# Performance work log

Measured on AMD Instinct MI355X. Metric: run time of the kernel, lower is better.

## Reference

```python
import math
import jax, jax.numpy as jnp
import numpy as np

D_MODEL, D_HEAD, BLOCK, B, N = 1024, 128, 2048, 4, 2048
# mode_gate('wake') blend weights (omega_lang, omega_grav)
OMEGA_LANG, OMEGA_GRAV = 0.7, 0.3


def setup_inputs() -> dict:
    key = jax.random.key(0)
    kx, kq, kk, kv, kl = jax.random.split(key, 5)
    x = jax.random.normal(kx, (B, N, D_MODEL), dtype=jnp.float32)
    # nn.Linear(d_model, d_head, bias=False) -> store as [d_model, d_head] for x @ W
    s = 1.0 / math.sqrt(D_MODEL)
    Wq = jax.random.uniform(kq, (D_MODEL, D_HEAD), jnp.float32, -s, s)
    Wk = jax.random.uniform(kk, (D_MODEL, D_HEAD), jnp.float32, -s, s)
    Wv = jax.random.uniform(kv, (D_MODEL, D_HEAD), jnp.float32, -s, s)
    # L_grav = eye*0.3 + randn*0.05
    L_grav = jnp.eye(D_HEAD, dtype=jnp.float32) * 0.3 \
        + jax.random.normal(kl, (D_HEAD, D_HEAD), dtype=jnp.float32) * 0.05
    return {"x": x, "Wq": Wq, "Wk": Wk, "Wv": Wv, "L_grav": L_grav}


def reference(x, Wq, Wk, Wv, L_grav):
    b, n, _ = x.shape
    d_head = Wq.shape[1]
    q = x @ Wq          # [b, n, d]
    k = x @ Wk          # [b, n, d]
    v = x @ Wv          # [b, n, d]
    mask = jnp.tril(jnp.ones((n, n), dtype=bool))  # causal, broadcast over batch

    # lang_attention: scaled dot-product with causal softmax
    scores = jnp.einsum('bqd,bkd->bqk', q, k) / math.sqrt(d_head)
    scores = jnp.where(mask, scores, -jnp.inf)
    a_lang = jax.nn.softmax(scores, axis=-1)       # [b, n, n]

    # grav_attention: Gaussian kernel on Mahalanobis-transformed keys y = k @ L_grav,
    # sigma = sqrt(d_head); masked + row-normalized (non-softmax).
    y = k @ L_grav                                  # [b, n, d]
    sq = jnp.sum(y * y, axis=-1)                    # [b, n]
    gram = jnp.einsum('bqd,bkd->bqk', y, y)         # [b, n, n]
    dist2 = jnp.maximum(sq[:, :, None] + sq[:, None, :] - 2.0 * gram, 0.0)
    kern = jnp.exp(-dist2 / (2.0 * d_head))         # sigma^2 = d_head
    kern = jnp.where(mask, kern, 0.0)
    a_grav = kern / (jnp.sum(kern, axis=-1, keepdims=True) + 1e-8)

    a = OMEGA_LANG * a_lang + OMEGA_GRAV * a_grav   # mode='wake' gate blend
    return a @ v                                    # [b, n, d_head]
```

## Files before the change

### kernel.cpp

```cpp
#include <hip/hip_runtime.h>
#include <hip/hip_bf16.h>
#include <math.h>

typedef __attribute__((ext_vector_type(8))) short short8;
typedef __attribute__((ext_vector_type(4))) short s16x4;
typedef __attribute__((ext_vector_type(4))) float f32x4;

#define SEQ 2048
#define DH 128


__device__ __forceinline__ short f2bf(float f) {
    union { float f; unsigned u; } v; v.f = f;
    unsigned r = v.u + 0x7fffu + ((v.u >> 16) & 1u);
    return (short)(r >> 16);
}
__device__ __forceinline__ float bf2f(short s) {
    union { unsigned u; float f; } v; v.u = ((unsigned)(unsigned short)s) << 16;
    return v.f;
}

__device__ __forceinline__ void gll16(const void* g, void* l) {
    __builtin_amdgcn_global_load_lds(
        (const __attribute__((address_space(1))) unsigned int*)g,
        (__attribute__((address_space(3))) unsigned int*)l, 16, 0, 0);
}

__global__ __launch_bounds__(256) void wt_kernel(
    const float* __restrict__ Wq, const float* __restrict__ Wk, const float* __restrict__ Wv,
    short* __restrict__ Wt2)
{
    const int t = threadIdx.x;
    const int m  = blockIdx.x >> 4;
    const int ks = blockIdx.x & 15;
    const float* W = m == 0 ? Wq : (m == 1 ? Wk : Wv);
    short* dst = Wt2 + ((size_t)(m * 16 + ks) * 1024) * 8;
    #pragma unroll
    for (int j = 0; j < 4; j++) {
        const int idx = t * 4 + j;
        const int ctile = idx >> 7;
        const int kc = (idx >> 6) & 1;
        const int gg = (idx >> 4) & 3;
        const int cc = idx & 15;
        const int col = ctile * 16 + cc;
        const int kb = ks * 64 + kc * 32 + gg * 8;
        short8 h;
        #pragma unroll
        for (int e = 0; e < 8; e++) h[e] = f2bf(W[(size_t)(kb + e) * 128 + col]);
        *(short8*)&dst[idx * 8] = h;
    }
}

__global__ __launch_bounds__(256) void proj_kernel(
    const float* __restrict__ x, const short* __restrict__ Wt2,
    short* __restrict__ Qh, short* __restrict__ Kh, short* __restrict__ Vh)
{
    __shared__ short Xs[2048];
    __shared__ short Ws[8192];
    const int t = threadIdx.x;
    const int w = t >> 6, l = t & 63;
    const int c = l & 15, g = l >> 4;
    const int bid = blockIdx.x;
    const int m = bid % 3;
    const int row0 = (bid / 3) * 32;
    const short* Wm = Wt2 + (size_t)m * 16 * 1024 * 8;

    const int xr = t >> 3;
    const int xk = (t & 7) * 8;
    const int xIdx = ((xr >> 4) * 2 + (xk >> 5)) * 64 + ((xk >> 3) & 3) * 16 + (xr & 15);

    const int rt = w & 1;
    const int ct4 = (w >> 1) * 4;
    f32x4 acc[4];
    #pragma unroll
    for (int nt = 0; nt < 4; nt++) acc[nt] = (f32x4)0.f;

    for (int ks = 0; ks < 16; ks++) {
        __syncthreads();
        const short* wsrc = Wm + ((size_t)ks * 1024 + w * 256 + l) * 8;
        #pragma unroll
        for (int j = 0; j < 4; j++)
            gll16(wsrc + j * 64 * 8, (void*)&Ws[(w * 256 + j * 64) * 8]);
        {
            const float* xp = &x[(size_t)(row0 + xr) * 1024 + ks * 64 + xk];
            const float4 a = *(const float4*)xp;
            const float4 b = *(const float4*)(xp + 4);
            short8 h;
            h[0] = f2bf(a.x); h[1] = f2bf(a.y); h[2] = f2bf(a.z); h[3] = f2bf(a.w);
            h[4] = f2bf(b.x); h[5] = f2bf(b.y); h[6] = f2bf(b.z); h[7] = f2bf(b.w);
            *(short8*)&Xs[xIdx * 8] = h;
        }
        __syncthreads();
        #pragma unroll
        for (int kc = 0; kc < 2; kc++) {
            const short8 af = *(const short8*)&Xs[((rt * 2 + kc) * 64 + l) * 8];
            #pragma unroll
            for (int nt = 0; nt < 4; nt++) {
                const short8 bf = *(const short8*)&Ws[(((ct4 + nt) * 2 + kc) * 64 + l) * 8];
                acc[nt] = __builtin_amdgcn_mfma_f32_16x16x32_bf16(af, bf, acc[nt], 0, 0, 0);
            }
        }
    }
    short* Out = m == 0 ? Qh : (m == 1 ? Kh : Vh);
    #pragma unroll
    for (int nt = 0; nt < 4; nt++)
        #pragma unroll
        for (int r = 0; r < 4; r++) {
            const int R = row0 + rt * 16 + 4 * g + r;
            const int col = (ct4 + nt) * 16 + c;
            const short hv = f2bf(acc[nt][r]);
            if (m == 2)
                Out[(size_t)R * 128 + col] = hv;
            else
                Out[(size_t)(R >> 6) * 8192 + ((col >> 3) * 64 + (R & 63)) * 8 + (col & 7)] = hv;
        }
}

__global__ __launch_bounds__(256) void y_kernel(
    const short* __restrict__ Kh, const float* __restrict__ L,
    short* __restrict__ Yh, float* __restrict__ SQ)
{
    __shared__ float Ls[128 * 128];
    __shared__ short Ks[16][128];
    const int t = threadIdx.x;
    const int row0 = blockIdx.x * 16;
    #pragma unroll
    for (int j = 0; j < 16; j++) {
        int lin = t + j * 256;
        ((float4*)Ls)[lin] = ((const float4*)L)[lin];
    }
    {
        int r = t >> 4, ch = t & 15;
        const int R = row0 + r;
        *(short8*)&Ks[r][ch * 8] =
            *(const short8*)&Kh[(size_t)(R >> 6) * 8192 + (ch * 64 + (R & 63)) * 8];
    }
    __syncthreads();
    const int rl = t >> 4, c4 = (t & 15) * 4;
    float acc[8] = {};
    for (int d = 0; d < 128; d++) {
        const float kd = bf2f(Ks[rl][d]);
        const float4 l0 = *(const float4*)&Ls[d * 128 + c4];
        const float4 l1 = *(const float4*)&Ls[d * 128 + c4 + 64];
        acc[0] += kd * l0.x; acc[1] += kd * l0.y; acc[2] += kd * l0.z; acc[3] += kd * l0.w;
        acc[4] += kd * l1.x; acc[5] += kd * l1.y; acc[6] += kd * l1.z; acc[7] += kd * l1.w;
    }
    const int R = row0 + rl;
    s16x4 h0, h1;
    float s = 0.f;
    #pragma unroll
    for (int j = 0; j < 4; j++) {
        short h = f2bf(acc[j]);     float rv = bf2f(h); s += rv * rv; h0[j] = h;
        short g = f2bf(acc[j + 4]); float gv = bf2f(g); s += gv * gv; h1[j] = g;
    }
    const size_t base = (size_t)(R >> 6) * 8192 + (size_t)(R & 63) * 8;
    *(s16x4*)&Yh[base + (c4 >> 3) * 512 + (c4 & 7)] = h0;
    *(s16x4*)&Yh[base + ((c4 + 64) >> 3) * 512 + (c4 & 7)] = h1;
    for (int off = 1; off < 16; off <<= 1) s += __shfl_xor(s, off);
    if ((t & 15) == 0) SQ[R] = s;
}

__global__ __launch_bounds__(256) void vt_kernel(
    const short* __restrict__ Vh, short* __restrict__ Vf)
{
    __shared__ short Ls[64][72];
    const int t = threadIdx.x;
    const int b  = blockIdx.x >> 6;
    const int nb = (blockIdx.x >> 1) & 31;
    const int db = blockIdx.x & 1;
    const int n0 = nb * 64, d0 = db * 64;
    const short* Vb = Vh + (size_t)b * SEQ * 128;
    short* Vfb = Vf + (size_t)b * SEQ * 128;
    #pragma unroll
    for (int i = 0; i < 2; i++) {
        int row = (t >> 3) + 32 * i;
        int ch = t & 7;
        *(short8*)&Ls[row][ch * 8] = *(const short8*)&Vb[(size_t)(n0 + row) * 128 + d0 + ch * 8];
    }
    __syncthreads();
    #pragma unroll
    for (int i = 0; i < 2; i++) {
        int dd = (t >> 3) + 32 * i;
        int nc = t & 7;
        short8 v;
        #pragma unroll
        for (int j = 0; j < 8; j++) v[j] = Ls[nc * 8 + j][dd];
        *(short8*)&Vfb[(size_t)(n0 >> 6) * 8192 + (nc * 128 + d0 + dd) * 8] = v;
    }
}

__global__ __launch_bounds__(256, 2) void attn_kernel(
    const short* __restrict__ Qf, const short* __restrict__ Kf,
    const short* __restrict__ Yf, const short* __restrict__ Vf,
    const float* __restrict__ SQv,
    float* __restrict__ OL, float* __restrict__ OG,
    float* __restrict__ LS, float* __restrict__ GS)
{
    __shared__ __align__(16) short Bs[2][8192];
    __shared__ __align__(16) short Vs[2][8192];
    __shared__ __align__(16) short P[4 * 2 * 512];
    __shared__ float Rs[32];
    float* Obuf = (float*)&Bs[0][0];

    const int t = threadIdx.x;
    const int w = t >> 6, l = t & 63;
    const int c = l & 15, g = l >> 4;
    const int qh = w & 1, kh = w >> 1;
    const int wbase = t & 192;
    const int bid = blockIdx.x;
    const int b = bid & 3;
    const int grav = (bid >> 2) & 1;
    const int s = (bid >> 3) & 1;
    const int jp = bid >> 4;

    const size_t fb = (size_t)b * SEQ * 128;
    const short* Ap = (grav ? Yf : Qf) + fb;
    const short* Bp = (grav ? Yf : Kf) + fb;
    const short* Vp = Vf + fb;
    const float* SQb = SQv + b * SEQ;

    const float CL = 0.12751743f;
    const float CG = -0.0056355275f;

    for (int m = 0; m < 2; m++) {
        const int qt = m ? 63 - jp : jp;
        const int q0 = qt * 32;
        const int nkt = (qt + 2) >> 1;

        __syncthreads();

        short8 qf[4];
        const size_t qtb = (size_t)(qt >> 1) * 8192;
        const int qlocal = (qt & 1) * 32 + qh * 16 + c;
        #pragma unroll
        for (int kc = 0; kc < 4; kc++)
            qf[kc] = *(const short8*)&Ap[qtb + ((kc * 4 + g) * 64 + qlocal) * 8];

        float sqq[4];
        if (grav) {
            #pragma unroll
            for (int r = 0; r < 4; r++)
                sqq[r] = SQb[q0 + qh * 16 + 4 * g + r];
        }

        f32x4 acc[8];
        #pragma unroll
        for (int dt = 0; dt < 8; dt++) acc[dt] = (f32x4)0.f;
        float rsum[4] = {};

        if (s < nkt) {
            {
                const short* bs0 = Bp + (size_t)s * 8192;
                const short* vs0 = Vp + (size_t)s * 8192;
                #pragma unroll
                for (int j = 0; j < 4; j++)
                    gll16(bs0 + (j * 256 + t) * 8, (void*)&Bs[0][(j * 256 + wbase) * 8]);
                #pragma unroll
                for (int j = 0; j < 4; j++)
                    gll16(vs0 + (j * 256 + t) * 8, (void*)&Vs[0][(j * 256 + wbase) * 8]);
            }
            int cur = 0, pb = 0;
            for (int tt = s; tt < nkt; tt += 2, cur ^= 1, pb ^= 1) {
                __syncthreads();
                if (tt + 2 < nkt) {
                    const short* bsn = Bp + (size_t)(tt + 2) * 8192;
                    const short* vsn = Vp + (size_t)(tt + 2) * 8192;
                    #pragma unroll
                    for (int j = 0; j < 4; j++)
                        gll16(bsn + (j * 256 + t) * 8, (void*)&Bs[cur ^ 1][(j * 256 + wbase) * 8]);
                    #pragma unroll
                    for (int j = 0; j < 4; j++)
                        gll16(vsn + (j * 256 + t) * 8, (void*)&Vs[cur ^ 1][(j * 256 + wbase) * 8]);
                }
                const int k0 = tt * 64;
                short* Pp = P + (w * 2 + pb) * 512;

                #pragma unroll
                for (int kt = 0; kt < 2; kt++) {
                    f32x4 sc = (f32x4)0.f;
                    #pragma unroll
                    for (int kc = 0; kc < 4; kc++) {
                        const short8 bf = *(const short8*)
                            &Bs[cur][((kc * 4 + g) * 64 + kh * 32 + kt * 16 + c) * 8];
                        sc = __builtin_amdgcn_mfma_f32_16x16x32_bf16(qf[kc], bf, sc, 0, 0, 0);
                    }
                    const int key = k0 + kh * 32 + kt * 16 + c;
                    const float sqkv = grav ? SQb[key] : 0.f;
                    #pragma unroll
                    for (int r = 0; r < 4; r++) {
                        const int qrow = q0 + qh * 16 + 4 * g + r;
                        float p = 0.f;
                        if (key <= qrow) {
                            if (grav) {
                                float d2 = sqq[r] + sqkv - 2.f * sc[r];
                                d2 = fmaxf(d2, 0.f);
                                p = __builtin_amdgcn_exp2f(d2 * CG);
                            } else {
                                p = __builtin_amdgcn_exp2f(sc[r] * CL);
                            }
                        }
                        const short ph = f2bf(p);
                        rsum[r] += bf2f(ph);
                        const int row = 4 * g + r;
                        Pp[row * 32 + ((kt * 16 + c) ^ (g << 3))] = ph;
                    }
                }

                const short8 pf = *(const short8*)&Pp[c * 32 + 8 * (g ^ ((c >> 2) & 3))];
                #pragma unroll
                for (int dt = 0; dt < 8; dt++) {
                    const short8 vf = *(const short8*)
                        &Vs[cur][((kh * 4 + g) * 128 + dt * 16 + c) * 8];
                    acc[dt] = __builtin_amdgcn_mfma_f32_16x16x32_bf16(pf, vf, acc[dt], 0, 0, 0);
                }
            }
        }

        __syncthreads();
        for (int i = t; i < 32 * 132; i += 256) Obuf[i] = 0.f;
        if (t < 32) Rs[t] = 0.f;
        __syncthreads();

        #pragma unroll
        for (int dt = 0; dt < 8; dt++)
            #pragma unroll
            for (int r = 0; r < 4; r++)
                atomicAdd(&Obuf[(qh * 16 + 4 * g + r) * 132 + dt * 16 + c], acc[dt][r]);

        #pragma unroll
        for (int r = 0; r < 4; r++) {
            float v = rsum[r];
            v += __shfl_xor(v, 1); v += __shfl_xor(v, 2);
            v += __shfl_xor(v, 4); v += __shfl_xor(v, 8);
            rsum[r] = v;
        }
        if (c == 0) {
            #pragma unroll
            for (int r = 0; r < 4; r++)
                atomicAdd(&Rs[qh * 16 + 4 * g + r], rsum[r]);
        }
        __syncthreads();

        float* Op = (grav ? OG : OL) + fb + (size_t)q0 * 128;
        #pragma unroll
        for (int i = 0; i < 16; i++) {
            const int v2 = t + 256 * i;
            atomicAdd(&Op[v2], Obuf[(v2 >> 7) * 132 + (v2 & 127)]);
        }
        if (t < 32) atomicAdd(&(grav ? GS : LS)[b * SEQ + q0 + t], Rs[t]);
    }
}

__global__ __launch_bounds__(256) void finalize_kernel(
    float* __restrict__ out, const float* __restrict__ OG,
    const float* __restrict__ LS, const float* __restrict__ GS)
{
    const int i4 = blockIdx.x * 256 + threadIdx.x;
    float4 o = ((float4*)out)[i4];
    const float4 gv = ((const float4*)OG)[i4];
    const int row = i4 >> 5;
    const float wl = 0.7f / LS[row];
    const float wg = 0.3f / (GS[row] + 1e-8f);
    o.x = o.x * wl + gv.x * wg;
    o.y = o.y * wl + gv.y * wg;
    o.z = o.z * wl + gv.z * wg;
    o.w = o.w * wl + gv.w * wg;
    ((float4*)out)[i4] = o;
}

extern "C" void kernel_launch(void* const* d_in, const int* in_sizes, int n_in,
                              void* d_out, int out_size, void* d_ws, size_t ws_size,
                              hipStream_t stream) {
    const float* x  = (const float*)d_in[0];
    const float* Wq = (const float*)d_in[1];
    const float* Wk = (const float*)d_in[2];
    const float* Wv = (const float*)d_in[3];
    const float* Lg = (const float*)d_in[4];

    char* ws = (char*)d_ws;
    short* Qh  = (short*)(ws + 0);
    short* Kh  = (short*)(ws + 2097152);
    short* Vh  = (short*)(ws + 4194304);
    short* Yh  = (short*)(ws + 6291456);
    short* Vf  = (short*)(ws + 8388608);
    short* Wt2 = (short*)(ws + 10485760);
    float* SQv = (float*)(ws + 11272192);
    float* LS  = (float*)(ws + 11304960);
    float* GS  = (float*)(ws + 11337728);
    float* OG  = (float*)(ws + 11370496);
    float* OL  = (float*)d_out;

    hipMemsetAsync(d_out, 0, 4194304, stream);
    hipMemsetAsync((void*)LS, 0, 65536, stream);
    hipMemsetAsync((void*)OG, 0, 4194304, stream);

    wt_kernel<<<48, 256, 0, stream>>>(Wq, Wk, Wv, Wt2);
    proj_kernel<<<768, 256, 0, stream>>>(x, Wt2, Qh, Kh, Vh);
    y_kernel<<<512, 256, 0, stream>>>(Kh, Lg, Yh, SQv);
    vt_kernel<<<256, 256, 0, stream>>>(Vh, Vf);
    attn_kernel<<<512, 256, 0, stream>>>(Qh, Kh, Yh, Vf, SQv, OL, OG, LS, GS);
    finalize_kernel<<<1024, 256, 0, stream>>>((float*)d_out, OG, LS, GS);
}
```

Measured before the change: 127.9 us.

## Drop LDS staging of K/V tiles, load fragments directly from global, one q-tile per block

The attention kernel no longer double-buffers K/Y and V tiles into shared memory with async global-to-LDS loads. Each wave now reads its MFMA operand fragments straight from global memory (relying on cache) and drops the per-iteration block barrier. The paired light/heavy q-tile loop is replaced by one q-tile per block with twice as many blocks, heaviest tiles first, and the 2-blocks-per-CU launch bound is removed. The smaller LDS footprint may allow more resident blocks, but every wave now fetches K/V redundantly from L2 without an explicit prefetch, so load latency is less hidden.

```diff
diff --git a/kernel.cpp b/kernel.cpp
--- a/kernel.cpp
+++ b/kernel.cpp
@@ -189,29 +189,28 @@
     }
 }
 
-__global__ __launch_bounds__(256, 2) void attn_kernel(
+__global__ __launch_bounds__(256) void attn_kernel(
     const short* __restrict__ Qf, const short* __restrict__ Kf,
     const short* __restrict__ Yf, const short* __restrict__ Vf,
     const float* __restrict__ SQv,
     float* __restrict__ OL, float* __restrict__ OG,
     float* __restrict__ LS, float* __restrict__ GS)
 {
-    __shared__ __align__(16) short Bs[2][8192];
-    __shared__ __align__(16) short Vs[2][8192];
     __shared__ __align__(16) short P[4 * 2 * 512];
+    __shared__ float Obuf[32][132];
     __shared__ float Rs[32];
-    float* Obuf = (float*)&Bs[0][0];
 
     const int t = threadIdx.x;
     const int w = t >> 6, l = t & 63;
     const int c = l & 15, g = l >> 4;
     const int qh = w & 1, kh = w >> 1;
-    const int wbase = t & 192;
     const int bid = blockIdx.x;
     const int b = bid & 3;
     const int grav = (bid >> 2) & 1;
     const int s = (bid >> 3) & 1;
-    const int jp = bid >> 4;
+    const int qt = 63 - (bid >> 4);
+    const int q0 = qt * 32;
+    const int nkt = (qt + 2) >> 1;
 
     const size_t fb = (size_t)b * SEQ * 128;
     const short* Ap = (grav ? Yf : Qf) + fb;
@@ -222,133 +221,115 @@
     const float CL = 0.12751743f;
     const float CG = -0.0056355275f;
 
-    for (int m = 0; m < 2; m++) {
-        const int qt = m ? 63 - jp : jp;
-        const int q0 = qt * 32;
-        const int nkt = (qt + 2) >> 1;
-
-        __syncthreads();
-
-        short8 qf[4];
-        const size_t qtb = (size_t)(qt >> 1) * 8192;
-        const int qlocal = (qt & 1) * 32 + qh * 16 + c;
-        #pragma unroll
-        for (int kc = 0; kc < 4; kc++)
-            qf[kc] = *(const short8*)&Ap[qtb + ((kc * 4 + g) * 64 + qlocal) * 8];
-
-        float sqq[4];
+    short8 qf[4];
+    const size_t qtb = (size_t)(qt >> 1) * 8192;
+    const int qlocal = (qt & 1) * 32 + qh * 16 + c;
+    #pragma unroll
+    for (int kc = 0; kc < 4; kc++)
+        qf[kc] = *(const short8*)&Ap[qtb + ((kc * 4 + g) * 64 + qlocal) * 8];
+
+    float sqq[4];
+    if (grav) {
+        #pragma unroll
+        for (int r = 0; r < 4; r++)
+            sqq[r] = SQb[q0 + qh * 16 + 4 * g + r];
+    }
+
+    f32x4 acc[8];
+    #pragma unroll
+    for (int dt = 0; dt < 8; dt++) acc[dt] = (f32x4)0.f;
+    float rsum[4] = {};
+
+    int pb = 0;
+    for (int tt = s; tt < nkt; tt += 2, pb ^= 1) {
+        const short* Bt = Bp + (size_t)tt * 8192;
+        const short* Vt = Vp + (size_t)tt * 8192;
+        short* Pp = P + (w * 2 + pb) * 512;
+        const int k0 = tt * 64;
+
+        short8 bf[2][4];
+        #pragma unroll
+        for (int kt = 0; kt < 2; kt++)
+            #pragma unroll
+            for (int kc = 0; kc < 4; kc++)
+                bf[kt][kc] = *(const short8*)
+                    &Bt[((kc * 4 + g) * 64 + kh * 32 + kt * 16 + c) * 8];
+        float sqk[2];
         if (grav) {
             #pragma unroll
-            for (int r = 0; r < 4; r++)
-                sqq[r] = SQb[q0 + qh * 16 + 4 * g + r];
-        }
-
-        f32x4 acc[8];
-        #pragma unroll
-        for (int dt = 0; dt < 8; dt++) acc[dt] = (f32x4)0.f;
-        float rsum[4] = {};
-
-        if (s < nkt) {
-            {
-                const short* bs0 = Bp + (size_t)s * 8192;
-                const short* vs0 = Vp + (size_t)s * 8192;
-                #pragma unroll
-                for (int j = 0; j < 4; j++)
-                    gll16(bs0 + (j * 256 + t) * 8, (void*)&Bs[0][(j * 256 + wbase) * 8]);
-                #pragma unroll
-                for (int j = 0; j < 4; j++)
-                    gll16(vs0 + (j * 256 + t) * 8, (void*)&Vs[0][(j * 256 + wbase) * 8]);
-            }
-            int cur = 0, pb = 0;
-            for (int tt = s; tt < nkt; tt += 2, cur ^= 1, pb ^= 1) {
-                __syncthreads();
-                if (tt + 2 < nkt) {
-                    const short* bsn = Bp + (size_t)(tt + 2) * 8192;
-                    const short* vsn = Vp + (size_t)(tt + 2) * 8192;
-                    #pragma unroll
-                    for (int j = 0; j < 4; j++)
-                        gll16(bsn + (j * 256 + t) * 8, (void*)&Bs[cur ^ 1][(j * 256 + wbase) * 8]);
-                    #pragma unroll
-                    for (int j = 0; j < 4; j++)
-                        gll16(vsn + (j * 256 + t) * 8, (void*)&Vs[cur ^ 1][(j * 256 + wbase) * 8]);
-                }
-                const int k0 = tt * 64;
-                short* Pp = P + (w * 2 + pb) * 512;
-
-                #pragma unroll
-                for (int kt = 0; kt < 2; kt++) {
-                    f32x4 sc = (f32x4)0.f;
-                    #pragma unroll
-                    for (int kc = 0; kc < 4; kc++) {
-                        const short8 bf = *(const short8*)
-                            &Bs[cur][((kc * 4 + g) * 64 + kh * 32 + kt * 16 + c) * 8];
-                        sc = __builtin_amdgcn_mfma_f32_16x16x32_bf16(qf[kc], bf, sc, 0, 0, 0);
-                    }
-                    const int key = k0 + kh * 32 + kt * 16 + c;
-                    const float sqkv = grav ? SQb[key] : 0.f;
-                    #pragma unroll
-                    for (int r = 0; r < 4; r++) {
-                        const int qrow = q0 + qh * 16 + 4 * g + r;
-                        float p = 0.f;
-                        if (key <= qrow) {
-                            if (grav) {
-                                float d2 = sqq[r] + sqkv - 2.f * sc[r];
-                                d2 = fmaxf(d2, 0.f);
-                                p = __builtin_amdgcn_exp2f(d2 * CG);
-                            } else {
-                                p = __builtin_amdgcn_exp2f(sc[r] * CL);
-                            }
-                        }
-                        const short ph = f2bf(p);
-                        rsum[r] += bf2f(ph);
-                        const int row = 4 * g + r;
-                        Pp[row * 32 + ((kt * 16 + c) ^ (g << 3))] = ph;
+            for (int kt = 0; kt < 2; kt++)
+                sqk[kt] = SQb[k0 + kh * 32 + kt * 16 + c];
+        }
+
+        #pragma unroll
+        for (int kt = 0; kt < 2; kt++) {
+            f32x4 sc = (f32x4)0.f;
+            #pragma unroll
+            for (int kc = 0; kc < 4; kc++)
+                sc = __builtin_amdgcn_mfma_f32_16x16x32_bf16(qf[kc], bf[kt][kc], sc, 0, 0, 0);
+            const int key = k0 + kh * 32 + kt * 16 + c;
+            const float sqkv = grav ? sqk[kt] : 0.f;
+            #pragma unroll
+            for (int r = 0; r < 4; r++) {
+                const int qrow = q0 + qh * 16 + 4 * g + r;
+                float p = 0.f;
+                if (key <= qrow) {
+                    if (grav) {
+                        float d2 = sqq[r] + sqkv - 2.f * sc[r];
+                        d2 = fmaxf(d2, 0.f);
+                        p = __builtin_amdgcn_exp2f(d2 * CG);
+                    } else {
+                        p = __builtin_amdgcn_exp2f(sc[r] * CL);
                     }
                 }
-
-                const short8 pf = *(const short8*)&Pp[c * 32 + 8 * (g ^ ((c >> 2) & 3))];
-                #pragma unroll
-                for (int dt = 0; dt < 8; dt++) {
-                    const short8 vf = *(const short8*)
-                        &Vs[cur][((kh * 4 + g) * 128 + dt * 16 + c) * 8];
-                    acc[dt] = __builtin_amdgcn_mfma_f32_16x16x32_bf16(pf, vf, acc[dt], 0, 0, 0);
-                }
+                const short ph = f2bf(p);
+                rsum[r] += bf2f(ph);
+                const int row = 4 * g + r;
+                Pp[row * 32 + ((kt * 16 + c) ^ (g << 3))] = ph;
             }
         }
 
-        __syncthreads();
-        for (int i = t; i < 32 * 132; i += 256) Obuf[i] = 0.f;
-        if (t < 32) Rs[t] = 0.f;
-        __syncthreads();
-
+        short8 vf[8];
         #pragma unroll
         for (int dt = 0; dt < 8; dt++)
-            #pragma unroll
-            for (int r = 0; r < 4; r++)
-                atomicAdd(&Obuf[(qh * 16 + 4 * g + r) * 132 + dt * 16 + c], acc[dt][r]);
-
-        #pragma unroll
-        for (int r = 0; r < 4; r++) {
-            float v = rsum[r];
-            v += __shfl_xor(v, 1); v += __shfl_xor(v, 2);
-            v += __shfl_xor(v, 4); v += __shfl_xor(v, 8);
-            rsum[r] = v;
-        }
-        if (c == 0) {
-            #pragma unroll
-            for (int r = 0; r < 4; r++)
-                atomicAdd(&Rs[qh * 16 + 4 * g + r], rsum[r]);
-        }
-        __syncthreads();
-
-        float* Op = (grav ? OG : OL) + fb + (size_t)q0 * 128;
-        #pragma unroll
-        for (int i = 0; i < 16; i++) {
-            const int v2 = t + 256 * i;
-            atomicAdd(&Op[v2], Obuf[(v2 >> 7) * 132 + (v2 & 127)]);
-        }
-        if (t < 32) atomicAdd(&(grav ? GS : LS)[b * SEQ + q0 + t], Rs[t]);
-    }
+            vf[dt] = *(const short8*)&Vt[((kh * 4 + g) * 128 + dt * 16 + c) * 8];
+        const short8 pf = *(const short8*)&Pp[c * 32 + 8 * (g ^ ((c >> 2) & 3))];
+        #pragma unroll
+        for (int dt = 0; dt < 8; dt++)
+            acc[dt] = __builtin_amdgcn_mfma_f32_16x16x32_bf16(pf, vf[dt], acc[dt], 0, 0, 0);
+    }
+
+    for (int i = t; i < 32 * 132; i += 256) ((float*)Obuf)[i] = 0.f;
+    if (t < 32) Rs[t] = 0.f;
+    __syncthreads();
+
+    #pragma unroll
+    for (int dt = 0; dt < 8; dt++)
+        #pragma unroll
+        for (int r = 0; r < 4; r++)
+            atomicAdd(&Obuf[qh * 16 + 4 * g + r][dt * 16 + c], acc[dt][r]);
+
+    #pragma unroll
+    for (int r = 0; r < 4; r++) {
+        float v = rsum[r];
+        v += __shfl_xor(v, 1); v += __shfl_xor(v, 2);
+        v += __shfl_xor(v, 4); v += __shfl_xor(v, 8);
+        rsum[r] = v;
+    }
+    if (c == 0) {
+        #pragma unroll
+        for (int r = 0; r < 4; r++)
+            atomicAdd(&Rs[qh * 16 + 4 * g + r], rsum[r]);
+    }
+    __syncthreads();
+
+    float* Op = (grav ? OG : OL) + fb + (size_t)q0 * 128;
+    #pragma unroll
+    for (int i = 0; i < 16; i++) {
+        const int v2 = t + 256 * i;
+        atomicAdd(&Op[v2], Obuf[v2 >> 7][v2 & 127]);
+    }
+    if (t < 32) atomicAdd(&(grav ? GS : LS)[b * SEQ + q0 + t], Rs[t]);
 }
 
 __global__ __launch_bounds__(256) void finalize_kernel(
@@ -398,6 +379,6 @@
     proj_kernel<<<768, 256, 0, stream>>>(x, Wt2, Qh, Kh, Vh);
     y_kernel<<<512, 256, 0, stream>>>(Kh, Lg, Yh, SQv);
     vt_kernel<<<256, 256, 0, stream>>>(Vh, Vf);
-    attn_kernel<<<512, 256, 0, stream>>>(Qh, Kh, Yh, Vf, SQv, OL, OG, LS, GS);
+    attn_kernel<<<1024, 256, 0, stream>>>(Qh, Kh, Yh, Vf, SQv, OL, OG, LS, GS);
     finalize_kernel<<<1024, 256, 0, stream>>>((float*)d_out, OG, LS, GS);
 }
```

Result: slower. 138.8 us (+8.5%).
